# Optimization experiments

Measured on AMD Instinct MI355X. Metric: run time of the kernel, lower is better.

## Reference

```python
import jax, jax.numpy as jnp
import numpy as np

N = 50000      # nodes
E = 800000     # edges (avg degree 16)
F_IN = 128
HID = 128
OUT = 64
K = 3          # TAGConv default number of hops


def setup_inputs() -> dict:
    key = jax.random.key(0)
    ks = jax.random.split(key, 4)
    x = jax.random.normal(ks[0], (N, F_IN), dtype=jnp.float32)
    edge_index = jax.random.randint(ks[1], (2, E), 0, N, dtype=jnp.int64)
    # K+1 per-hop linear weights per layer (Glorot-ish scale), plus biases
    W1 = jax.random.normal(ks[2], (K + 1, F_IN, HID), dtype=jnp.float32) / np.sqrt(F_IN)
    b1 = jnp.zeros((HID,), dtype=jnp.float32)
    W2 = jax.random.normal(ks[3], (K + 1, HID, OUT), dtype=jnp.float32) / np.sqrt(HID)
    b2 = jnp.zeros((OUT,), dtype=jnp.float32)
    return {"x": x, "edge_index": edge_index, "W1": W1, "b1": b1, "W2": W2, "b2": b2}


def _gcn_norm(edge_index, num_nodes):
    # Symmetric normalization D^{-1/2} A D^{-1/2}; TAGConv does NOT add self-loops.
    row, col = edge_index[0], edge_index[1]
    ones = jnp.ones((edge_index.shape[1],), dtype=jnp.float32)
    deg = jax.ops.segment_sum(ones, col, num_segments=num_nodes)  # in-degree at targets
    dinv = jnp.where(deg > 0, jax.lax.rsqrt(jnp.maximum(deg, 1.0)), 0.0)
    return dinv[row] * dinv[col]  # [E]


def _tagconv(x, edge_index, norm, W, b):
    # out = sum_{k=0..K} (A_norm^k x) @ W[k] + b
    row, col = edge_index[0], edge_index[1]
    n = x.shape[0]
    out = x @ W[0]
    h = x
    for k in range(1, W.shape[0]):
        # gather at sources, scale by edge norm, scatter-add at targets
        h = jax.ops.segment_sum(norm[:, None] * h[row], col, num_segments=n)
        out = out + h @ W[k]
    return out + b


def reference(x, edge_index, W1, b1, W2, b2):
    norm = _gcn_norm(edge_index, x.shape[0])
    h = jax.nn.relu(_tagconv(x, edge_index, norm, W1, b1))
    # dropout in eval mode is identity
    out = _tagconv(h, edge_index, norm, W2, b2)
    return jax.nn.log_softmax(out, axis=1)
```

## Files before the change

### kernel.cpp

```cpp
#include <hip/hip_runtime.h>
#include <math.h>


#define N_NODES 50000
#define N_EDGES 800000
#define NB_SCAN 196

typedef __attribute__((ext_vector_type(8))) short bf16x8;
typedef __attribute__((ext_vector_type(4))) float f32x4;

__device__ inline ushort f2b(float x) {
    unsigned u = __float_as_uint(x);
    return (ushort)((u + 0x7FFFu + ((u >> 16) & 1u)) >> 16);
}
__device__ inline float b2f(ushort b) { return __uint_as_float(((unsigned)b) << 16); }
__device__ inline float lo_f(unsigned u) { return __uint_as_float(u << 16); }
__device__ inline float hi_f(unsigned u) { return __uint_as_float(u & 0xFFFF0000u); }
__device__ inline unsigned pack2(float lo, float hi) {
    return ((unsigned)f2b(hi) << 16) | (unsigned)f2b(lo);
}


__global__ void count_deg_kernel(const int* __restrict__ col, int* __restrict__ deg, int e) {
    int i = blockIdx.x * 256 + threadIdx.x;
    if (i < e) atomicAdd(&deg[col[i]], 1);
}

__global__ void scan1_kernel(const int* __restrict__ deg, int* __restrict__ bsum,
                             float* __restrict__ dinv) {
    __shared__ int sd[256];
    int tid = threadIdx.x;
    int i = blockIdx.x * 256 + tid;
    int v = (i < N_NODES) ? deg[i] : 0;
    if (i < N_NODES) dinv[i] = (v > 0) ? (1.0f / sqrtf((float)v)) : 0.f;
    sd[tid] = v;
    __syncthreads();
    for (int o = 128; o > 0; o >>= 1) {
        if (tid < o) sd[tid] += sd[tid + o];
        __syncthreads();
    }
    if (tid == 0) bsum[blockIdx.x] = sd[0];
}

__global__ void scan2_kernel(int* __restrict__ bsum) {
    __shared__ int sd[256];
    int tid = threadIdx.x;
    int v = (tid < NB_SCAN) ? bsum[tid] : 0;
    sd[tid] = v;
    __syncthreads();
    for (int o = 1; o < 256; o <<= 1) {
        int t = (tid >= o) ? sd[tid - o] : 0;
        __syncthreads();
        sd[tid] += t;
        __syncthreads();
    }
    if (tid < NB_SCAN) bsum[tid] = sd[tid] - v;
}

__global__ void scan3_kernel(const int* __restrict__ deg, const int* __restrict__ bsum,
                             int* __restrict__ off, int* __restrict__ cursor) {
    __shared__ int sd[256];
    int tid = threadIdx.x;
    int i = blockIdx.x * 256 + tid;
    int v = (i < N_NODES) ? deg[i] : 0;
    sd[tid] = v;
    __syncthreads();
    for (int o = 1; o < 256; o <<= 1) {
        int t = (tid >= o) ? sd[tid - o] : 0;
        __syncthreads();
        sd[tid] += t;
        __syncthreads();
    }
    if (i < N_NODES) {
        int val = bsum[blockIdx.x] + sd[tid] - v;
        off[i] = val;
        cursor[i] = val;
    }
    if (i == N_NODES - 1) off[N_NODES] = N_EDGES;
}

__global__ void scatter_csr_kernel(const int* __restrict__ row, const int* __restrict__ col,
                                   const float* __restrict__ dinv, int* __restrict__ cursor,
                                   int2* __restrict__ meta, int e) {
    int i = blockIdx.x * 256 + threadIdx.x;
    if (i < e) {
        int r = row[i], c = col[i];
        int p = atomicAdd(&cursor[c], 1);
        float w = dinv[r] * dinv[c];
        meta[p] = make_int2(r, __float_as_int(w));
    }
}

__global__ void cvt_bf16_kernel(const float* __restrict__ src, ushort* __restrict__ dst) {
    int i = blockIdx.x * 256 + threadIdx.x;
    float4 v = ((const float4*)src)[i];
    ushort4 b;
    b.x = f2b(v.x); b.y = f2b(v.y); b.z = f2b(v.z); b.w = f2b(v.w);
    ((ushort4*)dst)[i] = b;
}

template <int NC>
__global__ void wtrans(const float* __restrict__ W, ushort* __restrict__ WT) {
    int idx = blockIdx.x * 256 + threadIdx.x;
    if (idx < 4 * 128 * NC) {
        int k = idx & 127;
        int hc = idx >> 7;
        int c = hc % NC;
        int hop = hc / NC;
        WT[idx] = f2b(W[((size_t)hop * 128 + k) * NC + c]);
    }
}

__global__ void prop128b(const ushort* __restrict__ h, const int* __restrict__ off,
                         const int2* __restrict__ meta, ushort* __restrict__ out) {
    int node = blockIdx.x * 4 + (threadIdx.x >> 6);
    int lane = threadIdx.x & 63;
    int s = __builtin_amdgcn_readfirstlane(off[node]);
    int e = __builtin_amdgcn_readfirstlane(off[node + 1]);
    const unsigned* h2 = (const unsigned*)h;

    float accx[4] = {0.f, 0.f, 0.f, 0.f};
    float accy[4] = {0.f, 0.f, 0.f, 0.f};
    int j = s;
    for (; j + 15 < e; j += 16) {
        int2 m[16];
        unsigned v[16];
#pragma unroll
        for (int u = 0; u < 16; ++u) m[u] = meta[j + u];
#pragma unroll
        for (int u = 0; u < 16; ++u) v[u] = h2[(size_t)m[u].x * 64 + lane];
#pragma unroll
        for (int u = 0; u < 16; ++u) {
            float w = __int_as_float(m[u].y);
            accx[u & 3] += w * lo_f(v[u]);
            accy[u & 3] += w * hi_f(v[u]);
        }
    }
    for (; j + 3 < e; j += 4) {
        int2 m[4];
        unsigned v[4];
#pragma unroll
        for (int u = 0; u < 4; ++u) m[u] = meta[j + u];
#pragma unroll
        for (int u = 0; u < 4; ++u) v[u] = h2[(size_t)m[u].x * 64 + lane];
#pragma unroll
        for (int u = 0; u < 4; ++u) {
            float w = __int_as_float(m[u].y);
            accx[u] += w * lo_f(v[u]);
            accy[u] += w * hi_f(v[u]);
        }
    }
    for (; j < e; ++j) {
        int2 m = meta[j];
        unsigned v = h2[(size_t)m.x * 64 + lane];
        float w = __int_as_float(m.y);
        accx[0] += w * lo_f(v);
        accy[0] += w * hi_f(v);
    }
    float rx = (accx[0] + accx[1]) + (accx[2] + accx[3]);
    float ry = (accy[0] + accy[1]) + (accy[2] + accy[3]);
    ((unsigned*)out)[(size_t)node * 64 + lane] = pack2(rx, ry);
}

template <int EPI>
__global__ void prop64b(const ushort* __restrict__ h, const int* __restrict__ off,
                        const int2* __restrict__ meta, const ushort* __restrict__ yadd,
                        const float* __restrict__ bias, void* __restrict__ outp) {
    int node = blockIdx.x * 4 + (threadIdx.x >> 6);
    int lane = threadIdx.x & 63;
    int s = __builtin_amdgcn_readfirstlane(off[node]);
    int e = __builtin_amdgcn_readfirstlane(off[node + 1]);

    float yv = b2f(yadd[(size_t)node * 64 + lane]);

    float acc[4] = {0.f, 0.f, 0.f, 0.f};
    int j = s;
    for (; j + 15 < e; j += 16) {
        int2 m[16];
        ushort v[16];
#pragma unroll
        for (int u = 0; u < 16; ++u) m[u] = meta[j + u];
#pragma unroll
        for (int u = 0; u < 16; ++u) v[u] = h[(size_t)m[u].x * 64 + lane];
#pragma unroll
        for (int u = 0; u < 16; ++u) acc[u & 3] += __int_as_float(m[u].y) * b2f(v[u]);
    }
    for (; j + 3 < e; j += 4) {
        int2 m[4];
        ushort v[4];
#pragma unroll
        for (int u = 0; u < 4; ++u) m[u] = meta[j + u];
#pragma unroll
        for (int u = 0; u < 4; ++u) v[u] = h[(size_t)m[u].x * 64 + lane];
#pragma unroll
        for (int u = 0; u < 4; ++u) acc[u] += __int_as_float(m[u].y) * b2f(v[u]);
    }
    for (; j < e; ++j) {
        int2 m = meta[j];
        acc[0] += __int_as_float(m.y) * b2f(h[(size_t)m.x * 64 + lane]);
    }
    float v = (acc[0] + acc[1]) + (acc[2] + acc[3]) + yv;
    if (EPI == 0) {
        ((ushort*)outp)[(size_t)node * 64 + lane] = f2b(v);
    } else {
        v += bias[lane];
        float m = v;
        for (int d = 32; d > 0; d >>= 1) m = fmaxf(m, __shfl_xor(m, d));
        float su = expf(v - m);
        for (int d = 32; d > 0; d >>= 1) su += __shfl_xor(su, d);
        ((float*)outp)[(size_t)node * 64 + lane] = (v - m) - logf(su);
    }
}

__device__ inline void stage_tile(ushort* hs, const ushort* hp, int row0, int tid) {
    const uint4* srcv = (const uint4*)(hp + (size_t)row0 * 128);
    for (int i = tid; i < 512; i += 256) {
        int r = i >> 4, c = i & 15;
        uint4 v = make_uint4(0, 0, 0, 0);
        if (row0 + r < N_NODES) v = srcv[i];
        int pc = c ^ (r & 7);
        *(uint4*)&hs[r * 128 + pc * 8] = v;
    }
}

__global__ __launch_bounds__(256) void mm_chain_mfma(
        const ushort* __restrict__ h0, const ushort* __restrict__ h1,
        const ushort* __restrict__ h2, const ushort* __restrict__ h3,
        const ushort* __restrict__ W1T,
        const float* __restrict__ bias, ushort* __restrict__ outp) {
    __shared__ ushort hs[32 * 128];
    const int tid = threadIdx.x;
    const int w = tid >> 6;
    const int lane = tid & 63;
    const int lrow = lane & 15;
    const int kgrp = lane >> 4;
    const int row0 = blockIdx.x * 32;

    f32x4 acc[2][2] = {};

#pragma unroll
    for (int hop = 0; hop < 4; ++hop) {
        const ushort* hp = (hop == 0) ? h0 : (hop == 1) ? h1 : (hop == 2) ? h2 : h3;
        if (hop) __syncthreads();
        stage_tile(hs, hp, row0, tid);
        __syncthreads();

#pragma unroll
        for (int kc = 0; kc < 4; ++kc) {
            bf16x8 a[2], b[2];
#pragma unroll
            for (int rt = 0; rt < 2; ++rt) {
                int row = rt * 16 + lrow;
                a[rt] = *(const bf16x8*)&hs[row * 128 + (((kc * 4 + kgrp) ^ (row & 7)) * 8)];
            }
#pragma unroll
            for (int ct = 0; ct < 2; ++ct) {
                int col = w * 32 + ct * 16 + lrow;
                b[ct] = *(const bf16x8*)&W1T[(((size_t)hop * 128 + col) << 7) + kc * 32 + kgrp * 8];
            }
#pragma unroll
            for (int rt = 0; rt < 2; ++rt)
#pragma unroll
                for (int ct = 0; ct < 2; ++ct)
                    acc[rt][ct] = __builtin_amdgcn_mfma_f32_16x16x32_bf16(
                        a[rt], b[ct], acc[rt][ct], 0, 0, 0);
        }
    }

#pragma unroll
    for (int rt = 0; rt < 2; ++rt)
#pragma unroll
        for (int ct = 0; ct < 2; ++ct) {
            int col = w * 32 + ct * 16 + lrow;
            float bv = bias[col];
#pragma unroll
            for (int i = 0; i < 4; ++i) {
                int row = row0 + rt * 16 + kgrp * 4 + i;
                if (row < N_NODES)
                    outp[(size_t)row * 128 + col] = f2b(fmaxf(acc[rt][ct][i] + bv, 0.f));
            }
        }
}

__global__ __launch_bounds__(256) void mm_y_mfma(
        const ushort* __restrict__ h,
        const ushort* __restrict__ W2T,
        ushort* __restrict__ y) {
    __shared__ ushort hs[32 * 128];
    const int tid = threadIdx.x;
    const int w = tid >> 6;
    const int lane = tid & 63;
    const int lrow = lane & 15;
    const int kgrp = lane >> 4;
    const int row0 = blockIdx.x * 32;

    f32x4 acc[2][4] = {};

    stage_tile(hs, h, row0, tid);
    __syncthreads();

#pragma unroll
    for (int kc = 0; kc < 4; ++kc) {
        bf16x8 a[2], b[4];
#pragma unroll
        for (int rt = 0; rt < 2; ++rt) {
            int row = rt * 16 + lrow;
            a[rt] = *(const bf16x8*)&hs[row * 128 + (((kc * 4 + kgrp) ^ (row & 7)) * 8)];
        }
#pragma unroll
        for (int ct = 0; ct < 4; ++ct) {
            int col = ct * 16 + lrow;
            b[ct] = *(const bf16x8*)&W2T[(((size_t)w * 64 + col) << 7) + kc * 32 + kgrp * 8];
        }
#pragma unroll
        for (int rt = 0; rt < 2; ++rt)
#pragma unroll
            for (int ct = 0; ct < 4; ++ct)
                acc[rt][ct] = __builtin_amdgcn_mfma_f32_16x16x32_bf16(
                    a[rt], b[ct], acc[rt][ct], 0, 0, 0);
    }

    ushort* yp = y + (size_t)w * N_NODES * 64;
#pragma unroll
    for (int rt = 0; rt < 2; ++rt)
#pragma unroll
        for (int ct = 0; ct < 4; ++ct) {
            int col = ct * 16 + lrow;
#pragma unroll
            for (int i = 0; i < 4; ++i) {
                int row = row0 + rt * 16 + kgrp * 4 + i;
                if (row < N_NODES)
                    yp[(size_t)row * 64 + col] = f2b(acc[rt][ct][i]);
            }
        }
}


extern "C" void kernel_launch(void* const* d_in, const int* in_sizes, int n_in,
                              void* d_out, int out_size, void* d_ws, size_t ws_size,
                              hipStream_t stream) {
    const float* x  = (const float*)d_in[0];
    const int*   ei = (const int*)d_in[1];
    const float* W1 = (const float*)d_in[2];
    const float* b1 = (const float*)d_in[3];
    const float* W2 = (const float*)d_in[4];
    const float* b2 = (const float*)d_in[5];
    float* out = (float*)d_out;

    const int* row = ei;
    const int* col = ei + N_EDGES;

    char* ws_base = (char*)d_ws;
    size_t o = 0;
    auto carve = [&](size_t bytes) {
        void* p = ws_base + o;
        o = (o + bytes + 511) & ~(size_t)511;
        return p;
    };
    int*    deg    = (int*)carve(N_NODES * 4);
    float*  dinv   = (float*)carve(N_NODES * 4);
    int*    off    = (int*)carve((N_NODES + 1) * 4);
    int*    cursor = (int*)carve(N_NODES * 4);
    int*    bsum   = (int*)carve(NB_SCAN * 4);
    int2*   meta   = (int2*)carve((size_t)N_EDGES * 8);
    ushort* W1T    = (ushort*)carve(4 * 128 * 128 * 2);
    ushort* W2T    = (ushort*)carve(4 * 64 * 128 * 2);
    ushort* xb     = (ushort*)carve((size_t)N_NODES * 128 * 2);
    ushort* A      = (ushort*)carve((size_t)N_NODES * 128 * 2);
    ushort* B      = (ushort*)carve((size_t)N_NODES * 128 * 2);
    ushort* C      = (ushort*)carve((size_t)N_NODES * 128 * 2);
    ushort* hid    = (ushort*)carve((size_t)N_NODES * 128 * 2);
    ushort* y2     = (ushort*)carve((size_t)4 * N_NODES * 64 * 2);
    ushort* T2     = (ushort*)carve((size_t)N_NODES * 64 * 2);

    ushort* y2_0 = y2;
    ushort* y2_1 = y2 + (size_t)1 * N_NODES * 64;
    ushort* y2_2 = y2 + (size_t)2 * N_NODES * 64;
    ushort* y2_3 = y2 + (size_t)3 * N_NODES * 64;
    ushort* S2   = y2_3;

    const int nb_e = (N_EDGES + 255) / 256;

    wtrans<128><<<256, 256, 0, stream>>>(W1, W1T);
    wtrans<64><<<128, 256, 0, stream>>>(W2, W2T);
    cvt_bf16_kernel<<<6250, 256, 0, stream>>>(x, xb);

    hipMemsetAsync(deg, 0, N_NODES * 4, stream);
    count_deg_kernel<<<nb_e, 256, 0, stream>>>(col, deg, N_EDGES);
    scan1_kernel<<<NB_SCAN, 256, 0, stream>>>(deg, bsum, dinv);
    scan2_kernel<<<1, 256, 0, stream>>>(bsum);
    scan3_kernel<<<NB_SCAN, 256, 0, stream>>>(deg, bsum, off, cursor);
    scatter_csr_kernel<<<nb_e, 256, 0, stream>>>(row, col, dinv, cursor, meta, N_EDGES);

    prop128b<<<12500, 256, 0, stream>>>(xb, off, meta, A);
    prop128b<<<12500, 256, 0, stream>>>(A,  off, meta, B);
    prop128b<<<12500, 256, 0, stream>>>(B,  off, meta, C);
    mm_chain_mfma<<<1563, 256, 0, stream>>>(xb, A, B, C, W1T, b1, hid);

    mm_y_mfma<<<1563, 256, 0, stream>>>(hid, W2T, y2);
    prop64b<0><<<12500, 256, 0, stream>>>(y2_3, off, meta, y2_2, nullptr, T2);
    prop64b<0><<<12500, 256, 0, stream>>>(T2,   off, meta, y2_1, nullptr, S2);
    prop64b<2><<<12500, 256, 0, stream>>>(S2,   off, meta, y2_0, b2,      out);
}
```

Before: 376.8 us.

## Build CSR via two-pass bucketed scatter and merge conversion kernels

Replaces the per-edge global atomic scatter into CSR with a two-stage scheme. Edges are first binned into 32-node buckets using global atomics on bucket cursors, packing (src,dst) into 16-bit halves. Then each block places its bucket's edges using shared-memory atomics and computes the edge weights there. The weight transposes and the x-to-bf16 conversion are also merged into one launch. This adds an extra pass and an intermediate buffer, and the 16-bit packing relies on node ids staying below 65536.

```diff
diff --git a/kernel.cpp b/kernel.cpp
--- a/kernel.cpp
+++ b/kernel.cpp
@@ -5,6 +5,7 @@
 #define N_NODES 50000
 #define N_EDGES 800000
 #define NB_SCAN 196
+#define NBUCK   1563
 
 typedef __attribute__((ext_vector_type(8))) short bf16x8;
 typedef __attribute__((ext_vector_type(4))) float f32x4;
@@ -58,7 +59,7 @@
 }
 
 __global__ void scan3_kernel(const int* __restrict__ deg, const int* __restrict__ bsum,
-                             int* __restrict__ off, int* __restrict__ cursor) {
+                             int* __restrict__ off, int* __restrict__ bcur) {
     __shared__ int sd[256];
     int tid = threadIdx.x;
     int i = blockIdx.x * 256 + tid;
@@ -74,40 +75,72 @@
     if (i < N_NODES) {
         int val = bsum[blockIdx.x] + sd[tid] - v;
         off[i] = val;
-        cursor[i] = val;
+        if ((i & 31) == 0) bcur[i >> 5] = val;
     }
     if (i == N_NODES - 1) off[N_NODES] = N_EDGES;
 }
 
-__global__ void scatter_csr_kernel(const int* __restrict__ row, const int* __restrict__ col,
-                                   const float* __restrict__ dinv, int* __restrict__ cursor,
-                                   int2* __restrict__ meta, int e) {
+__global__ void bin_scatter_kernel(const int* __restrict__ row, const int* __restrict__ col,
+                                   int* __restrict__ bcur, unsigned* __restrict__ binned,
+                                   int e) {
     int i = blockIdx.x * 256 + threadIdx.x;
     if (i < e) {
         int r = row[i], c = col[i];
-        int p = atomicAdd(&cursor[c], 1);
-        float w = dinv[r] * dinv[c];
-        meta[p] = make_int2(r, __float_as_int(w));
-    }
-}
-
-__global__ void cvt_bf16_kernel(const float* __restrict__ src, ushort* __restrict__ dst) {
-    int i = blockIdx.x * 256 + threadIdx.x;
-    float4 v = ((const float4*)src)[i];
-    ushort4 b;
-    b.x = f2b(v.x); b.y = f2b(v.y); b.z = f2b(v.z); b.w = f2b(v.w);
-    ((ushort4*)dst)[i] = b;
-}
-
-template <int NC>
-__global__ void wtrans(const float* __restrict__ W, ushort* __restrict__ WT) {
-    int idx = blockIdx.x * 256 + threadIdx.x;
-    if (idx < 4 * 128 * NC) {
+        int p = atomicAdd(&bcur[c >> 5], 1);
+        binned[p] = ((unsigned)r << 16) | (unsigned)c;
+    }
+}
+
+__global__ void csr_place_kernel(const unsigned* __restrict__ binned,
+                                 const int* __restrict__ off,
+                                 const float* __restrict__ dinv,
+                                 int2* __restrict__ meta) {
+    __shared__ int lcur[32];
+    const int b = blockIdx.x;
+    const int n0 = b * 32;
+    const int nend = min(n0 + 32, N_NODES);
+    const int tid = threadIdx.x;
+    if (tid < 32) {
+        int n = n0 + tid;
+        lcur[tid] = (n < N_NODES) ? off[n] : 0;
+    }
+    __syncthreads();
+    const int base = off[n0];
+    const int cnt = off[nend] - base;
+    for (int i = tid; i < cnt; i += 256) {
+        unsigned ec = binned[base + i];
+        int src = (int)(ec >> 16);
+        int c = (int)(ec & 0xFFFFu);
+        int p = atomicAdd(&lcur[c - n0], 1);
+        float w = dinv[src] * dinv[c];
+        meta[p] = make_int2(src, __float_as_int(w));
+    }
+}
+
+__global__ void convert_kernel(const float* __restrict__ W1, const float* __restrict__ W2,
+                               const float* __restrict__ x, ushort* __restrict__ W1T,
+                               ushort* __restrict__ W2T, ushort* __restrict__ xb) {
+    int bid = blockIdx.x;
+    if (bid < 256) {
+        int idx = bid * 256 + threadIdx.x;
         int k = idx & 127;
         int hc = idx >> 7;
-        int c = hc % NC;
-        int hop = hc / NC;
-        WT[idx] = f2b(W[((size_t)hop * 128 + k) * NC + c]);
+        int c = hc & 127;
+        int hop = hc >> 7;
+        W1T[idx] = f2b(W1[(((size_t)hop * 128 + k) << 7) | c]);
+    } else if (bid < 384) {
+        int idx = (bid - 256) * 256 + threadIdx.x;
+        int k = idx & 127;
+        int hc = idx >> 7;
+        int c = hc & 63;
+        int hop = hc >> 6;
+        W2T[idx] = f2b(W2[(((size_t)hop * 128 + k) << 6) | c]);
+    } else {
+        int i = (bid - 384) * 256 + threadIdx.x;
+        float4 v = ((const float4*)x)[i];
+        ushort4 bb;
+        bb.x = f2b(v.x); bb.y = f2b(v.y); bb.z = f2b(v.z); bb.w = f2b(v.w);
+        ((ushort4*)xb)[i] = bb;
     }
 }
 
@@ -357,21 +390,22 @@
         o = (o + bytes + 511) & ~(size_t)511;
         return p;
     };
-    int*    deg    = (int*)carve(N_NODES * 4);
-    float*  dinv   = (float*)carve(N_NODES * 4);
-    int*    off    = (int*)carve((N_NODES + 1) * 4);
-    int*    cursor = (int*)carve(N_NODES * 4);
-    int*    bsum   = (int*)carve(NB_SCAN * 4);
-    int2*   meta   = (int2*)carve((size_t)N_EDGES * 8);
-    ushort* W1T    = (ushort*)carve(4 * 128 * 128 * 2);
-    ushort* W2T    = (ushort*)carve(4 * 64 * 128 * 2);
-    ushort* xb     = (ushort*)carve((size_t)N_NODES * 128 * 2);
-    ushort* A      = (ushort*)carve((size_t)N_NODES * 128 * 2);
-    ushort* B      = (ushort*)carve((size_t)N_NODES * 128 * 2);
-    ushort* C      = (ushort*)carve((size_t)N_NODES * 128 * 2);
-    ushort* hid    = (ushort*)carve((size_t)N_NODES * 128 * 2);
-    ushort* y2     = (ushort*)carve((size_t)4 * N_NODES * 64 * 2);
-    ushort* T2     = (ushort*)carve((size_t)N_NODES * 64 * 2);
+    int*      deg    = (int*)carve(N_NODES * 4);
+    float*    dinv   = (float*)carve(N_NODES * 4);
+    int*      off    = (int*)carve((N_NODES + 1) * 4);
+    int*      bsum   = (int*)carve(NB_SCAN * 4);
+    int*      bcur   = (int*)carve(NBUCK * 4);
+    unsigned* binned = (unsigned*)carve((size_t)N_EDGES * 4);
+    int2*     meta   = (int2*)carve((size_t)N_EDGES * 8);
+    ushort*   W1T    = (ushort*)carve(4 * 128 * 128 * 2);
+    ushort*   W2T    = (ushort*)carve(4 * 64 * 128 * 2);
+    ushort*   xb     = (ushort*)carve((size_t)N_NODES * 128 * 2);
+    ushort*   A      = (ushort*)carve((size_t)N_NODES * 128 * 2);
+    ushort*   B      = (ushort*)carve((size_t)N_NODES * 128 * 2);
+    ushort*   C      = (ushort*)carve((size_t)N_NODES * 128 * 2);
+    ushort*   hid    = (ushort*)carve((size_t)N_NODES * 128 * 2);
+    ushort*   y2     = (ushort*)carve((size_t)4 * N_NODES * 64 * 2);
+    ushort*   T2     = (ushort*)carve((size_t)N_NODES * 64 * 2);
 
     ushort* y2_0 = y2;
     ushort* y2_1 = y2 + (size_t)1 * N_NODES * 64;
@@ -381,16 +415,15 @@
 
     const int nb_e = (N_EDGES + 255) / 256;
 
-    wtrans<128><<<256, 256, 0, stream>>>(W1, W1T);
-    wtrans<64><<<128, 256, 0, stream>>>(W2, W2T);
-    cvt_bf16_kernel<<<6250, 256, 0, stream>>>(x, xb);
+    convert_kernel<<<6634, 256, 0, stream>>>(W1, W2, x, W1T, W2T, xb);
 
     hipMemsetAsync(deg, 0, N_NODES * 4, stream);
     count_deg_kernel<<<nb_e, 256, 0, stream>>>(col, deg, N_EDGES);
     scan1_kernel<<<NB_SCAN, 256, 0, stream>>>(deg, bsum, dinv);
     scan2_kernel<<<1, 256, 0, stream>>>(bsum);
-    scan3_kernel<<<NB_SCAN, 256, 0, stream>>>(deg, bsum, off, cursor);
-    scatter_csr_kernel<<<nb_e, 256, 0, stream>>>(row, col, dinv, cursor, meta, N_EDGES);
+    scan3_kernel<<<NB_SCAN, 256, 0, stream>>>(deg, bsum, off, bcur);
+    bin_scatter_kernel<<<nb_e, 256, 0, stream>>>(row, col, bcur, binned, N_EDGES);
+    csr_place_kernel<<<NBUCK, 256, 0, stream>>>(binned, off, dinv, meta);
 
     prop128b<<<12500, 256, 0, stream>>>(xb, off, meta, A);
     prop128b<<<12500, 256, 0, stream>>>(A,  off, meta, B);
```

Result: slower. 464.2 us (+23.2%).
